# Kernel optimization log

Hardware: AMD Instinct MI355X
Metric: run time of the kernel (lower is better)

Reference implementation:

```python
import jax, jax.numpy as jnp
import numpy as np

B, H, W = 8, 56, 56
DIM_IN = 1792 + 2   # concatenated pyramid channels + 2 coord channels
D_OUT = 1792 // 4   # gamma_d = 4
N_CENTERS = H * W   # gamma_c = 1
K = 3


def avg_pool3(x):
    # F.avg_pool2d(x, 3, 1, 1) with count_include_pad=True: padded sum / 9
    s = jax.lax.reduce_window(x, 0.0, jax.lax.add, (1, 1, 3, 3), (1, 1, 1, 1),
                              ((0, 0), (0, 0), (1, 1), (1, 1)))
    return s / 9.0


def setup_inputs() -> dict:
    key = jax.random.key(0)
    k0, k1, k2, kw, kb, kc = jax.random.split(key, 6)
    p0 = jax.random.normal(k0, (B, 256, H, W), dtype=jnp.float32)
    p1 = jax.random.normal(k1, (B, 512, 28, 28), dtype=jnp.float32)
    p2 = jax.random.normal(k2, (B, 1024, 14, 14), dtype=jnp.float32)
    conv_w = jax.random.normal(kw, (D_OUT, DIM_IN), dtype=jnp.float32) * 0.02
    conv_b = jax.random.normal(kb, (D_OUT,), dtype=jnp.float32) * 0.01
    C = jax.random.normal(kc, (D_OUT, N_CENTERS), dtype=jnp.float32) * 0.5
    return {"p0": p0, "p1": p1, "p2": p2, "conv_w": conv_w, "conv_b": conv_b, "C": C}


def reference(p0, p1, p2, conv_w, conv_b, C):
    # Descriptor: avg-pool each level, upsample to first level, concat channels
    o0 = avg_pool3(p0)
    o1 = avg_pool3(p1)
    o2 = avg_pool3(p2)
    o1 = jax.image.resize(o1, (B, o1.shape[1], H, W), method='bilinear')  # align_corners=False equiv (upsample)
    o2 = jax.image.resize(o2, (B, o2.shape[1], H, W), method='bilinear')
    sample = jnp.concatenate([o0, o1, o2], axis=1)  # (B, 1792, H, W)

    # AddCoords: xx = row index / (H-1), yy = col index / (W-1), both *2-1
    xx = (jnp.arange(H, dtype=jnp.float32) / (H - 1) * 2 - 1)[:, None] * jnp.ones((1, W), jnp.float32)
    yy = (jnp.arange(W, dtype=jnp.float32) / (W - 1) * 2 - 1)[None, :] * jnp.ones((H, 1), jnp.float32)
    coords = jnp.broadcast_to(jnp.stack([xx, yy])[None], (B, 2, H, W))
    sample = jnp.concatenate([sample, coords], axis=1)  # (B, 1794, H, W)

    # 1x1 CoordConv
    phi = jnp.einsum('bchw,oc->bohw', sample, conv_w) + conv_b[None, :, None, None]
    phi_p = phi.transpose(0, 2, 3, 1).reshape(B, H * W, D_OUT)  # b (h w) c

    # squared distance to center bank via norm expansion
    feat2 = jnp.sum(phi_p ** 2, axis=2, keepdims=True)        # (B, HW, 1)
    cent2 = jnp.sum(C ** 2, axis=0)[None, None, :]            # (1, 1, N)
    dist = jnp.sqrt(feat2 + cent2 - 2.0 * jnp.matmul(phi_p, C))  # (B, HW, N)

    # top-K smallest, ascending
    neg_top, _ = jax.lax.top_k(-dist, K)
    topv = -neg_top                                           # (B, HW, K) ascending
    soft = jax.nn.softmax(-topv, axis=-1)                     # softmin
    score = soft[:, :, 0] * topv[:, :, 0]                     # (B, HW)
    return score.reshape(B, 1, H, W)
```

## Files before the change

### kernel.cpp

```cpp
#include <hip/hip_runtime.h>
#include <math.h>

#define B_    8
#define H_    56
#define W_    56
#define HW_   3136
#define C0_   256
#define C1_   512
#define C2_   1024
#define DIN_  1794
#define KD_   1792
#define KCP_  56
#define DOUT_ 448
#define NCHP_ 28
#define NC_   3136
#define NCHD_ 196
#define KCD_  14
#define DTS_  452
#define PCH_  28672

typedef __attribute__((ext_vector_type(8))) short bh8;
typedef __attribute__((ext_vector_type(4))) float f32x4;

__device__ __forceinline__ short f2bf(float f) {
  union { float f; unsigned u; } v; v.f = f;
  unsigned r = v.u + 0x7fffu + ((v.u >> 16) & 1u);
  return (short)(r >> 16);
}
__device__ __forceinline__ float bf2f(short s) {
  union { unsigned u; float f; } v; v.u = ((unsigned)(unsigned short)s) << 16;
  return v.f;
}

__global__ __launch_bounds__(256) void desc0_kernel(const float* __restrict__ p0,
                                                    short* __restrict__ desc) {
  __shared__ float sv[64 * 57];
  const int c0 = blockIdx.x * 64, h = blockIdx.y, b = blockIdx.z;
  for (int item = threadIdx.x; item < 64 * 56; item += 256) {
    int x = item % 56, c = item / 56;
    const float* src = p0 + (((size_t)(b * C0_ + c0 + c)) * 56 + h) * 56 + x;
    float s = src[0];
    if (h > 0)  s += src[-56];
    if (h < 55) s += src[56];
    sv[c * 57 + x] = s;
  }
  __syncthreads();
  for (int item = threadIdx.x; item < 56 * 8; item += 256) {
    int g = item & 7, w = item >> 3;
    bh8 o;
#pragma unroll
    for (int j = 0; j < 8; ++j) {
      const float* s0 = sv + (g * 8 + j) * 57;
      float v = s0[w];
      if (w > 0)  v += s0[w - 1];
      if (w < 55) v += s0[w + 1];
      o[j] = f2bf(v * (1.0f / 9.0f));
    }
    size_t pid = (size_t)b * HW_ + h * 56 + w;
    *(bh8*)(desc + pid * KD_ + c0 + g * 8) = o;
  }
}

__global__ __launch_bounds__(256) void desc1_kernel(const float* __restrict__ p1,
                                                    short* __restrict__ desc) {
  __shared__ float sv[2 * 64 * 29];
  const int c0 = blockIdx.x * 64, h = blockIdx.y, b = blockIdx.z;
  float sy = (h + 0.5f) * 0.5f - 0.5f;
  float fyf = floorf(sy);
  float fy = sy - fyf;
  int iy = (int)fyf;
  int pya = min(max(iy, 0), 27), pyb = min(max(iy + 1, 0), 27);
  for (int item = threadIdx.x; item < 64 * 2 * 28; item += 256) {
    int x = item % 28;
    int pr = (item / 28) & 1;
    int c = item / 56;
    int r = pr ? pyb : pya;
    const float* src = p1 + (((size_t)(b * C1_ + c0 + c)) * 28 + r) * 28 + x;
    float s = src[0];
    if (r > 0)  s += src[-28];
    if (r < 27) s += src[28];
    sv[pr * (64 * 29) + c * 29 + x] = s;
  }
  __syncthreads();
  for (int item = threadIdx.x; item < 56 * 8; item += 256) {
    int g = item & 7, w = item >> 3;
    float sx = (w + 0.5f) * 0.5f - 0.5f;
    float fxf = floorf(sx);
    float fx = sx - fxf;
    int ix = (int)fxf;
    int x0 = min(max(ix, 0), 27), x1 = min(max(ix + 1, 0), 27);
    bh8 o;
#pragma unroll
    for (int j = 0; j < 8; ++j) {
      const float* s0 = sv + (g * 8 + j) * 29;
      const float* s1 = s0 + 64 * 29;
      float p00 = s0[x0] + (x0 > 0 ? s0[x0 - 1] : 0.f) + (x0 < 27 ? s0[x0 + 1] : 0.f);
      float p01 = s0[x1] + (x1 > 0 ? s0[x1 - 1] : 0.f) + (x1 < 27 ? s0[x1 + 1] : 0.f);
      float p10 = s1[x0] + (x0 > 0 ? s1[x0 - 1] : 0.f) + (x0 < 27 ? s1[x0 + 1] : 0.f);
      float p11 = s1[x1] + (x1 > 0 ? s1[x1 - 1] : 0.f) + (x1 < 27 ? s1[x1 + 1] : 0.f);
      float top = p00 + fx * (p01 - p00);
      float bot = p10 + fx * (p11 - p10);
      o[j] = f2bf((top + fy * (bot - top)) * (1.0f / 9.0f));
    }
    size_t pid = (size_t)b * HW_ + h * 56 + w;
    *(bh8*)(desc + pid * KD_ + C0_ + c0 + g * 8) = o;
  }
}

__global__ __launch_bounds__(256) void desc2_kernel(const float* __restrict__ p2,
                                                    short* __restrict__ desc) {
  __shared__ float sv[2 * 64 * 15];
  const int c0 = blockIdx.x * 64, h = blockIdx.y, b = blockIdx.z;
  float sy = (h + 0.5f) * 0.25f - 0.5f;
  float fyf = floorf(sy);
  float fy = sy - fyf;
  int iy = (int)fyf;
  int pya = min(max(iy, 0), 13), pyb = min(max(iy + 1, 0), 13);
  for (int item = threadIdx.x; item < 64 * 2 * 14; item += 256) {
    int x = item % 14;
    int pr = (item / 14) & 1;
    int c = item / 28;
    int r = pr ? pyb : pya;
    const float* src = p2 + (((size_t)(b * C2_ + c0 + c)) * 14 + r) * 14 + x;
    float s = src[0];
    if (r > 0)  s += src[-14];
    if (r < 13) s += src[14];
    sv[pr * (64 * 15) + c * 15 + x] = s;
  }
  __syncthreads();
  for (int item = threadIdx.x; item < 56 * 8; item += 256) {
    int g = item & 7, w = item >> 3;
    float sx = (w + 0.5f) * 0.25f - 0.5f;
    float fxf = floorf(sx);
    float fx = sx - fxf;
    int ix = (int)fxf;
    int x0 = min(max(ix, 0), 13), x1 = min(max(ix + 1, 0), 13);
    bh8 o;
#pragma unroll
    for (int j = 0; j < 8; ++j) {
      const float* s0 = sv + (g * 8 + j) * 15;
      const float* s1 = s0 + 64 * 15;
      float p00 = s0[x0] + (x0 > 0 ? s0[x0 - 1] : 0.f) + (x0 < 13 ? s0[x0 + 1] : 0.f);
      float p01 = s0[x1] + (x1 > 0 ? s0[x1 - 1] : 0.f) + (x1 < 13 ? s0[x1 + 1] : 0.f);
      float p10 = s1[x0] + (x0 > 0 ? s1[x0 - 1] : 0.f) + (x0 < 13 ? s1[x0 + 1] : 0.f);
      float p11 = s1[x1] + (x1 > 0 ? s1[x1 - 1] : 0.f) + (x1 < 13 ? s1[x1 + 1] : 0.f);
      float top = p00 + fx * (p01 - p00);
      float bot = p10 + fx * (p11 - p10);
      o[j] = f2bf((top + fy * (bot - top)) * (1.0f / 9.0f));
    }
    size_t pid = (size_t)b * HW_ + h * 56 + w;
    *(bh8*)(desc + pid * KD_ + C0_ + C1_ + c0 + g * 8) = o;
  }
}

__global__ void cent2_kernel(const float* __restrict__ C, float* __restrict__ c2) {
  int j = blockIdx.x * blockDim.x + threadIdx.x;
  if (j >= NC_) return;
  float s = 0.f;
  for (int d = 0; d < DOUT_; ++d) {
    float v = bf2f(f2bf(C[(size_t)d * NC_ + j]));
    s = fmaf(v, v, s);
  }
  c2[j] = s;
}

__global__ void cpack_kernel(const float* __restrict__ C, short* __restrict__ Cpk) {
  int idx = blockIdx.x * 256 + threadIdx.x;
  int ln = idx & 63;
  int kc = (idx >> 6) % KCD_;
  int nc = idx / (KCD_ * 64);
  int n  = nc * 16 + (ln & 15);
  int k0 = kc * 32 + ((ln >> 4) << 3);
  bh8 o;
#pragma unroll
  for (int j = 0; j < 8; ++j) o[j] = f2bf(C[(size_t)(k0 + j) * NC_ + n]);
  *(bh8*)(Cpk + (size_t)idx * 8) = o;
}

__global__ void wpack_kernel(const float* __restrict__ W, short* __restrict__ Wpk) {
  int idx = blockIdx.x * 256 + threadIdx.x;
  int ln = idx & 63;
  int kc = (idx >> 6) % KCP_;
  int nc = idx / (KCP_ * 64);
  int n  = nc * 16 + (ln & 15);
  int k0 = kc * 32 + ((ln >> 4) << 3);
  bh8 o;
#pragma unroll
  for (int j = 0; j < 8; ++j) o[j] = f2bf(W[(size_t)n * DIN_ + k0 + j]);
  *(bh8*)(Wpk + (size_t)idx * 8) = o;
}

__global__ __launch_bounds__(256) void phi_mfma(
    const short* __restrict__ desc, const short* __restrict__ Wpk,
    const float* __restrict__ cw, const float* __restrict__ cb,
    short* __restrict__ phip ) {
  __shared__ __align__(16) float Dt[16 * DTS_];
  const int wv = threadIdx.x >> 6, ln = threadIdx.x & 63;
  const int pix0 = blockIdx.x * 32;
  const short* aptr = desc + ((size_t)(pix0 + (ln & 15))) * KD_ + ((ln >> 4) << 3);

  f32x4 acc[2][7];
#pragma unroll
  for (int rc = 0; rc < 2; ++rc)
#pragma unroll
    for (int i = 0; i < 7; ++i) acc[rc][i] = (f32x4){0.f, 0.f, 0.f, 0.f};

  const short* bbase = Wpk + (size_t)(wv * 7) * (KCP_ * 512) + ln * 8;
  for (int kc = 0; kc < KCP_; ++kc) {
    bh8 a0 = *(const bh8*)(aptr + kc * 32);
    bh8 a1 = *(const bh8*)(aptr + 16 * KD_ + kc * 32);
    const short* bp = bbase + kc * 512;
#pragma unroll
    for (int i = 0; i < 7; ++i) {
      bh8 bfr = *(const bh8*)(bp + (size_t)i * (KCP_ * 512));
      acc[0][i] = __builtin_amdgcn_mfma_f32_16x16x32_bf16(a0, bfr, acc[0][i], 0, 0, 0);
      acc[1][i] = __builtin_amdgcn_mfma_f32_16x16x32_bf16(a1, bfr, acc[1][i], 0, 0, 0);
    }
  }

  for (int rc = 0; rc < 2; ++rc) {
    __syncthreads();
#pragma unroll
    for (int i = 0; i < 7; ++i) {
      int col = (wv * 7 + i) * 16 + (ln & 15);
      float bias = cb[col];
      float wx = cw[(size_t)col * DIN_ + 1792];
      float wy = cw[(size_t)col * DIN_ + 1793];
#pragma unroll
      for (int r = 0; r < 4; ++r) {
        int row = ((ln >> 4) << 2) + r;
        int pid = pix0 + rc * 16 + row;
        int hw = pid % HW_;
        int hh = hw / 56, ww = hw % 56;
        float xx = (float)hh * (2.0f / 55.0f) - 1.0f;
        float yy = (float)ww * (2.0f / 55.0f) - 1.0f;
        Dt[row * DTS_ + col] = acc[rc][i][r] + bias + wx * xx + wy * yy;
      }
    }
    __syncthreads();
    short* op = phip + (size_t)(blockIdx.x * 2 + rc) * PCH_;
    for (int item = threadIdx.x; item < KCD_ * 64; item += 256) {
      int kc = item >> 6, lp = item & 63;
      int m = lp & 15, k0 = kc * 32 + ((lp >> 4) << 3);
      bh8 o;
#pragma unroll
      for (int j = 0; j < 8; ++j) o[j] = f2bf(Dt[m * DTS_ + k0 + j]);
      *(bh8*)(op + (size_t)item * 8) = o;
    }
  }
}

__device__ __forceinline__ void insert3(float& t0, float& t1, float& t2, float v) {
  if (v < t2) {
    if (v < t1) {
      t2 = t1;
      if (v < t0) { t1 = t0; t0 = v; } else t1 = v;
    } else t2 = v;
  }
}
__device__ __forceinline__ void merge3(float& a0, float& a1, float& a2,
                                       float b0, float b1, float b2) {
  float lo0 = fminf(a0, b0), hi0 = fmaxf(a0, b0);
  float lo1 = fminf(a1, b1), hi1 = fmaxf(a1, b1);
  float lo2 = fminf(a2, b2);
  a0 = lo0;
  a1 = fminf(hi0, lo1);
  a2 = fminf(fmaxf(hi0, lo1), fminf(hi1, lo2));
}

__global__ __launch_bounds__(256) void dist_part(
    const short* __restrict__ phip, const short* __restrict__ Cpk,
    const float* __restrict__ c2g, float* __restrict__ part) {
  const int wv = threadIdx.x >> 6, ln = threadIdx.x & 63;
  const int chunk = blockIdx.x;

  bh8 A[KCD_];
  const short* ap = phip + (size_t)chunk * PCH_ + ln * 8;
#pragma unroll
  for (int kc = 0; kc < KCD_; ++kc) A[kc] = *(const bh8*)(ap + kc * 512);

  float sum = 0.f;
#pragma unroll
  for (int kc = 0; kc < KCD_; ++kc)
#pragma unroll
    for (int j = 0; j < 8; ++j) { float v = bf2f(A[kc][j]); sum = fmaf(v, v, sum); }
  sum += __shfl_xor(sum, 16, 64);
  sum += __shfl_xor(sum, 32, 64);
  float f2r[4];
#pragma unroll
  for (int r = 0; r < 4; ++r) f2r[r] = __shfl(sum, ((ln >> 4) << 2) + r, 64);

  float t3[4][3];
#pragma unroll
  for (int r = 0; r < 4; ++r) { t3[r][0] = 1e30f; t3[r][1] = 1e30f; t3[r][2] = 1e30f; }

  const short* bbase = Cpk + (size_t)(wv * 49) * (KCD_ * 512) + ln * 8;
  for (int i = 0; i < 49; ++i) {
    const short* bp = bbase + (size_t)i * (KCD_ * 512);
    f32x4 acc = {0.f, 0.f, 0.f, 0.f};
#pragma unroll
    for (int kc = 0; kc < KCD_; ++kc) {
      bh8 b = *(const bh8*)(bp + kc * 512);
      acc = __builtin_amdgcn_mfma_f32_16x16x32_bf16(A[kc], b, acc, 0, 0, 0);
    }
    int nc = wv * 49 + i;
    float c2v = c2g[nc * 16 + (ln & 15)];
#pragma unroll
    for (int r = 0; r < 4; ++r)
      insert3(t3[r][0], t3[r][1], t3[r][2], f2r[r] + c2v - 2.0f * acc[r]);
  }

#pragma unroll
  for (int m = 1; m <= 8; m <<= 1) {
#pragma unroll
    for (int r = 0; r < 4; ++r) {
      float b0 = __shfl_xor(t3[r][0], m, 64);
      float b1 = __shfl_xor(t3[r][1], m, 64);
      float b2 = __shfl_xor(t3[r][2], m, 64);
      merge3(t3[r][0], t3[r][1], t3[r][2], b0, b1, b2);
    }
  }

  if ((ln & 15) == 0) {
#pragma unroll
    for (int r = 0; r < 4; ++r) {
      int row = ((ln >> 4) << 2) + r;
      float* q = part + ((size_t)(chunk * 16 + row)) * 16 + wv * 4;
      q[0] = t3[r][0];
      q[1] = t3[r][1];
      q[2] = t3[r][2];
    }
  }
}

__global__ __launch_bounds__(256) void merge_kernel(const float* __restrict__ part,
                                                    float* __restrict__ out) {
  int p = blockIdx.x * 256 + threadIdx.x;
  const float* q = part + (size_t)p * 16;
  float a0 = q[0], a1 = q[1], a2 = q[2];
#pragma unroll
  for (int w = 1; w < 4; ++w) merge3(a0, a1, a2, q[w * 4], q[w * 4 + 1], q[w * 4 + 2]);
  float d0 = sqrtf(fmaxf(a0, 0.f));
  float d1 = sqrtf(fmaxf(a1, 0.f));
  float d2 = sqrtf(fmaxf(a2, 0.f));
  float s0 = 1.0f / (1.0f + expf(d0 - d1) + expf(d0 - d2));
  out[p] = s0 * d0;
}

extern "C" void kernel_launch(void* const* d_in, const int* in_sizes, int n_in,
                              void* d_out, int out_size, void* d_ws, size_t ws_size,
                              hipStream_t stream) {
  const float* p0 = (const float*)d_in[0];
  const float* p1 = (const float*)d_in[1];
  const float* p2 = (const float*)d_in[2];
  const float* cw = (const float*)d_in[3];
  const float* cb = (const float*)d_in[4];
  const float* C  = (const float*)d_in[5];
  float* out = (float*)d_out;

  short* desc = (short*)d_ws;
  short* Cpk  = desc + (size_t)25088 * KD_;
  short* Wpk  = Cpk + (size_t)NCHD_ * KCD_ * 512;
  float* c2   = (float*)(Wpk + (size_t)NCHP_ * KCP_ * 512);
  float* part = c2 + NC_;

  desc0_kernel<<<dim3(4, 56, 8),  256, 0, stream>>>(p0, desc);
  desc1_kernel<<<dim3(8, 56, 8),  256, 0, stream>>>(p1, desc);
  desc2_kernel<<<dim3(16, 56, 8), 256, 0, stream>>>(p2, desc);
  cent2_kernel<<<(NC_ + 255) / 256, 256, 0, stream>>>(C, c2);
  cpack_kernel<<<NCHD_ * KCD_ * 64 / 256, 256, 0, stream>>>(C, Cpk);
  wpack_kernel<<<NCHP_ * KCP_ * 64 / 256, 256, 0, stream>>>(cw, Wpk);
  phi_mfma<<<25088 / 32, 256, 0, stream>>>(desc, Wpk, cw, cb, desc);
  dist_part<<<25088 / 16, 256, 0, stream>>>(desc, Cpk, c2, part);
  merge_kernel<<<25088 / 256, 256, 0, stream>>>(part, out);
}
```

Baseline: 703.7 us.

## Split distance block into two row chunks, each wave covering half the centers

Each block of the distance kernel now handles two 16-row chunks. Each pair of waves splits the 196 center chunks in half, and each wave processes two center chunks per iteration with two independent MFMA accumulators. This halves the partial top-3 storage and the merge work, and adds MFMA instruction-level parallelism. In exchange, each wave streams twice as much of the center bank, and per-block reuse of B tiles across waves changes.

```diff
diff --git a/kernel.cpp b/kernel.cpp
--- a/kernel.cpp
+++ b/kernel.cpp
@@ -272,7 +272,8 @@
     const short* __restrict__ phip, const short* __restrict__ Cpk,
     const float* __restrict__ c2g, float* __restrict__ part) {
   const int wv = threadIdx.x >> 6, ln = threadIdx.x & 63;
-  const int chunk = blockIdx.x;
+  const int chunk = blockIdx.x * 2 + (wv >> 1);
+  const int half  = wv & 1;
 
   bh8 A[KCD_];
   const short* ap = phip + (size_t)chunk * PCH_ + ln * 8;
@@ -294,20 +295,27 @@
 #pragma unroll
   for (int r = 0; r < 4; ++r) { t3[r][0] = 1e30f; t3[r][1] = 1e30f; t3[r][2] = 1e30f; }
 
-  const short* bbase = Cpk + (size_t)(wv * 49) * (KCD_ * 512) + ln * 8;
-  for (int i = 0; i < 49; ++i) {
-    const short* bp = bbase + (size_t)i * (KCD_ * 512);
-    f32x4 acc = {0.f, 0.f, 0.f, 0.f};
+  const int nc0 = half * (NCHD_ / 2);
+  const short* bbase = Cpk + (size_t)nc0 * (KCD_ * 512) + ln * 8;
+  for (int i = 0; i < NCHD_ / 4; ++i) {
+    int ncA = i * 2, ncB = i * 2 + 1;
+    const short* bpA = bbase + (size_t)ncA * (KCD_ * 512);
+    const short* bpB = bbase + (size_t)ncB * (KCD_ * 512);
+    f32x4 accA = {0.f, 0.f, 0.f, 0.f}, accB = {0.f, 0.f, 0.f, 0.f};
 #pragma unroll
     for (int kc = 0; kc < KCD_; ++kc) {
-      bh8 b = *(const bh8*)(bp + kc * 512);
-      acc = __builtin_amdgcn_mfma_f32_16x16x32_bf16(A[kc], b, acc, 0, 0, 0);
-    }
-    int nc = wv * 49 + i;
-    float c2v = c2g[nc * 16 + (ln & 15)];
-#pragma unroll
-    for (int r = 0; r < 4; ++r)
-      insert3(t3[r][0], t3[r][1], t3[r][2], f2r[r] + c2v - 2.0f * acc[r]);
+      bh8 bA = *(const bh8*)(bpA + kc * 512);
+      bh8 bB = *(const bh8*)(bpB + kc * 512);
+      accA = __builtin_amdgcn_mfma_f32_16x16x32_bf16(A[kc], bA, accA, 0, 0, 0);
+      accB = __builtin_amdgcn_mfma_f32_16x16x32_bf16(A[kc], bB, accB, 0, 0, 0);
+    }
+    float c2A = c2g[(nc0 + ncA) * 16 + (ln & 15)];
+    float c2B = c2g[(nc0 + ncB) * 16 + (ln & 15)];
+#pragma unroll
+    for (int r = 0; r < 4; ++r) {
+      insert3(t3[r][0], t3[r][1], t3[r][2], f2r[r] + c2A - 2.0f * accA[r]);
+      insert3(t3[r][0], t3[r][1], t3[r][2], f2r[r] + c2B - 2.0f * accB[r]);
+    }
   }
 
 #pragma unroll
@@ -325,7 +333,7 @@
 #pragma unroll
     for (int r = 0; r < 4; ++r) {
       int row = ((ln >> 4) << 2) + r;
-      float* q = part + ((size_t)(chunk * 16 + row)) * 16 + wv * 4;
+      float* q = part + ((size_t)(chunk * 16 + row)) * 8 + half * 4;
       q[0] = t3[r][0];
       q[1] = t3[r][1];
       q[2] = t3[r][2];
@@ -336,10 +344,9 @@
 __global__ __launch_bounds__(256) void merge_kernel(const float* __restrict__ part,
                                                     float* __restrict__ out) {
   int p = blockIdx.x * 256 + threadIdx.x;
-  const float* q = part + (size_t)p * 16;
+  const float* q = part + (size_t)p * 8;
   float a0 = q[0], a1 = q[1], a2 = q[2];
-#pragma unroll
-  for (int w = 1; w < 4; ++w) merge3(a0, a1, a2, q[w * 4], q[w * 4 + 1], q[w * 4 + 2]);
+  merge3(a0, a1, a2, q[4], q[5], q[6]);
   float d0 = sqrtf(fmaxf(a0, 0.f));
   float d1 = sqrtf(fmaxf(a1, 0.f));
   float d2 = sqrtf(fmaxf(a2, 0.f));
@@ -371,6 +378,6 @@
   cpack_kernel<<<NCHD_ * KCD_ * 64 / 256, 256, 0, stream>>>(C, Cpk);
   wpack_kernel<<<NCHP_ * KCP_ * 64 / 256, 256, 0, stream>>>(cw, Wpk);
   phi_mfma<<<25088 / 32, 256, 0, stream>>>(desc, Wpk, cw, cb, desc);
-  dist_part<<<25088 / 16, 256, 0, stream>>>(desc, Cpk, c2, part);
+  dist_part<<<25088 / 32, 256, 0, stream>>>(desc, Cpk, c2, part);
   merge_kernel<<<25088 / 256, 256, 0, stream>>>(part, out);
 }
```

Measured after the change: 699.6 us. Within noise of the previous version (-0.6%).
